# Kernel tuning notes

Hardware: AMD Instinct MI355X
Metric: run time of the kernel (lower is better)

The kernel has to match this reference:

```python
import jax, jax.numpy as jnp
import numpy as np

D_MODEL = 512
OUT_MODEL = 512
NUM_HEADS = 8
D_K = OUT_MODEL // NUM_HEADS


def setup_inputs() -> dict:
    key = jax.random.key(0)
    ks = jax.random.split(key, 11)
    B, S = 4, 2048
    inp = {
        "Q": jax.random.normal(ks[0], (B, S, D_MODEL), dtype=jnp.float32),
        "K": jax.random.normal(ks[1], (B, S, D_MODEL), dtype=jnp.float32),
        "V": jax.random.normal(ks[2], (B, S, D_MODEL), dtype=jnp.float32),
    }
    sc = 1.0 / np.sqrt(D_MODEL)
    inp["Wq"] = jax.random.normal(ks[3], (D_MODEL, OUT_MODEL), dtype=jnp.float32) * sc
    inp["bq"] = jnp.zeros((OUT_MODEL,), dtype=jnp.float32)
    inp["Wk"] = jax.random.normal(ks[4], (D_MODEL, OUT_MODEL), dtype=jnp.float32) * sc
    inp["bk"] = jnp.zeros((OUT_MODEL,), dtype=jnp.float32)
    inp["Wv"] = jax.random.normal(ks[5], (D_MODEL, OUT_MODEL), dtype=jnp.float32) * sc
    inp["bv"] = jnp.zeros((OUT_MODEL,), dtype=jnp.float32)
    inp["Wo"] = jax.random.normal(ks[6], (OUT_MODEL, OUT_MODEL), dtype=jnp.float32) * sc
    inp["bo"] = jnp.zeros((OUT_MODEL,), dtype=jnp.float32)
    return inp


def _split_heads(x):
    B, S, _ = x.shape
    return x.reshape(B, S, NUM_HEADS, D_K).transpose(0, 2, 1, 3)  # [B,H,S,Dk]


def reference(Q, K, V, Wq, bq, Wk, bk, Wv, bv, Wo, bo):
    q = _split_heads(Q @ Wq + bq)
    k = _split_heads(K @ Wk + bk)
    v = _split_heads(V @ Wv + bv)
    scores = jnp.einsum("bhsd,bhtd->bhst", q, k) / jnp.sqrt(jnp.float32(D_K))
    probs = jax.nn.softmax(scores, axis=-1)
    attn = jnp.einsum("bhst,bhtd->bhsd", probs, v)  # [B,H,S,Dk]
    B, H, S, Dk = attn.shape
    merged = attn.transpose(0, 2, 1, 3).reshape(B, S, OUT_MODEL)
    return merged @ Wo + bo
```

## Files before the change

### kernel.cpp

```cpp
#include <hip/hip_runtime.h>
#include <hip/hip_bf16.h>
#include <cstdint>


using short8 = __attribute__((ext_vector_type(8))) short;
using f32x4  = __attribute__((ext_vector_type(4))) float;
using f32x16 = __attribute__((ext_vector_type(16))) float;

#define DEVINL __device__ __forceinline__

constexpr int BB  = 4;
constexpr int SS  = 2048;
constexpr int DM  = 512;
constexpr int NH  = 8;
constexpr int DKH = 64;
constexpr float C2 = 0.18033688011112042f;

DEVINL unsigned short f2bf(float f) {
    __hip_bfloat16 h = __float2bfloat16(f);
    return *reinterpret_cast<unsigned short*>(&h);
}

DEVINL f32x4 mfma16(short8 a, short8 b, f32x4 c) {
    return __builtin_amdgcn_mfma_f32_16x16x32_bf16(a, b, c, 0, 0, 0);
}
DEVINL f32x16 mfma32(short8 a, short8 b, f32x16 c) {
    return __builtin_amdgcn_mfma_f32_32x32x16_bf16(a, b, c, 0, 0, 0);
}

DEVINL void gl16(const void* g, void* l) {
    __builtin_amdgcn_global_load_lds(
        (const __attribute__((address_space(1))) unsigned int*)g,
        (__attribute__((address_space(3))) unsigned int*)l, 16, 0, 0);
}
DEVINL void vmcnt0() { asm volatile("s_waitcnt vmcnt(0)" ::: "memory"); }

DEVINL unsigned cvtpk(float a, float b) {
    unsigned r;
    asm("v_cvt_pk_bf16_f32 %0, %1, %2" : "=v"(r) : "v"(a), "v"(b));
    return r;
}

__global__ __launch_bounds__(256)
void prep_w(const float* __restrict__ Wq, const float* __restrict__ Wk,
            const float* __restrict__ Wv, const float* __restrict__ Wo,
            unsigned short* __restrict__ wt)
{
    const int z = blockIdx.z;
    const float* W = (z == 0) ? Wq : (z == 1) ? Wk : (z == 2) ? Wv : Wo;
    unsigned short* Wtz = wt + (size_t)z * DM * DM;

    __shared__ unsigned short T[64][72];
    const int t = threadIdx.x;
    const int k0 = blockIdx.x * 64, n0 = blockIdx.y * 64;
    const int r = t >> 2, cs = t & 3;

    #pragma unroll
    for (int q = 0; q < 4; ++q) {
        float4 v = *reinterpret_cast<const float4*>(
            &W[(size_t)(k0 + r) * DM + n0 + cs * 16 + q * 4]);
        union { unsigned short u[4]; unsigned long long ll; } pk;
        pk.u[0] = f2bf(v.x); pk.u[1] = f2bf(v.y);
        pk.u[2] = f2bf(v.z); pk.u[3] = f2bf(v.w);
        *reinterpret_cast<unsigned long long*>(&T[r][cs * 16 + q * 4]) = pk.ll;
    }
    __syncthreads();
    union { unsigned short u[8]; short8 v; } p0, p1;
    #pragma unroll
    for (int e = 0; e < 8; ++e) p0.u[e] = T[cs * 16 + e][r];
    #pragma unroll
    for (int e = 0; e < 8; ++e) p1.u[e] = T[cs * 16 + 8 + e][r];
    *reinterpret_cast<short8*>(&Wtz[(size_t)(n0 + r) * DM + k0 + cs * 16]) = p0.v;
    *reinterpret_cast<short8*>(&Wtz[(size_t)(n0 + r) * DM + k0 + cs * 16 + 8]) = p1.v;
}

__global__ __launch_bounds__(256, 4)
void qkv_proj_kernel(const float* __restrict__ Qin, const float* __restrict__ Kin,
                     const float* __restrict__ Vin,
                     const unsigned short* __restrict__ wt,
                     const float* __restrict__ bq, const float* __restrict__ bk,
                     const float* __restrict__ bv,
                     unsigned short* __restrict__ qb, unsigned short* __restrict__ kb2,
                     unsigned short* __restrict__ vt2)
{
    const int z = blockIdx.z;
    const float* A           = (z == 0) ? Qin : (z == 1) ? Kin : Vin;
    const unsigned short* Wt = wt + (size_t)z * DM * DM;
    const float* bias        = (z == 0) ? bq : (z == 1) ? bk : bv;

    __shared__ unsigned short SMEM[16384];

    const int tid = threadIdx.x, lane = tid & 63, w = tid >> 6;
    const int wm = w >> 1, wn = w & 1;
    const int row16 = lane & 15, kg = lane >> 4;
    const int m0tok = blockIdx.x * 128, n0ch = blockIdx.y * 128;

    const int ar = tid >> 1, ah = tid & 1;

    float4 apf[4];
    auto load_A = [&](int kt) {
        const float* Ap = &A[(size_t)(m0tok + ar) * DM + kt * 32 + ah * 16];
        #pragma unroll
        for (int q = 0; q < 4; ++q)
            apf[q] = *reinterpret_cast<const float4*>(Ap + q * 4);
    };
    auto write_A = [&](int buf) {
        #pragma unroll
        for (int s = 0; s < 2; ++s) {
            union { unsigned short u[8]; short8 v; } pk;
            float4 a = apf[2 * s], b = apf[2 * s + 1];
            pk.u[0] = f2bf(a.x); pk.u[1] = f2bf(a.y);
            pk.u[2] = f2bf(a.z); pk.u[3] = f2bf(a.w);
            pk.u[4] = f2bf(b.x); pk.u[5] = f2bf(b.y);
            pk.u[6] = f2bf(b.z); pk.u[7] = f2bf(b.w);
            int phys = (ah * 2 + s) ^ (ar & 3);
            *reinterpret_cast<short8*>(&SMEM[buf * 4096 + ar * 32 + phys * 8]) = pk.v;
        }
    };
    auto issue_B = [&](int kt, int buf) {
        #pragma unroll
        for (int i = 0; i < 2; ++i) {
            int chunk = tid + i * 256;
            int n = chunk >> 2, c = chunk & 3;
            const unsigned short* src =
                &Wt[(size_t)(n0ch + n) * DM + kt * 32 + ((c ^ (n & 3)) * 8)];
            gl16(src, (char*)SMEM + 16384 + (size_t)buf * 8192 +
                      (size_t)(w * 64 + i * 256) * 16);
        }
    };

    f32x4 acc[4][4] = {};
    const int aoff = ((z == 2) ? wn : wm) * 64;
    const int boff = ((z == 2) ? wm : wn) * 64;

    load_A(0); issue_B(0, 0);
    vmcnt0();
    write_A(0);
    __syncthreads();

    for (int t = 0; t < 16; ++t) {
        const int cur = t & 1, nxt = cur ^ 1;
        if (t + 1 < 16) { issue_B(t + 1, nxt); load_A(t + 1); }

        short8 af[4], bfr[4];
        #pragma unroll
        for (int i = 0; i < 4; ++i) {
            int ra = aoff + i * 16 + row16;
            int rb = boff + i * 16 + row16;
            af[i]  = *reinterpret_cast<const short8*>(
                &SMEM[cur * 4096 + ra * 32 + ((kg ^ (ra & 3)) * 8)]);
            bfr[i] = *reinterpret_cast<const short8*>(
                &SMEM[8192 + cur * 4096 + rb * 32 + ((kg ^ (rb & 3)) * 8)]);
        }
        __builtin_amdgcn_s_setprio(1);
        #pragma unroll
        for (int mf = 0; mf < 4; ++mf)
            #pragma unroll
            for (int nf = 0; nf < 4; ++nf)
                acc[mf][nf] = (z == 2)
                    ? mfma16(bfr[mf], af[nf], acc[mf][nf])
                    : mfma16(af[mf], bfr[nf], acc[mf][nf]);
        __builtin_amdgcn_s_setprio(0);

        vmcnt0();
        if (t + 1 < 16) write_A(nxt);
        __syncthreads();
    }

    if (z == 0) {
        #pragma unroll
        for (int nf = 0; nf < 4; ++nf) {
            int ch = n0ch + wn * 64 + nf * 16 + row16;
            float bval = bias[ch];
            int h = ch >> 6, dk = ch & 63;
            #pragma unroll
            for (int mf = 0; mf < 4; ++mf)
                #pragma unroll
                for (int j = 0; j < 4; ++j) {
                    int tok = m0tok + wm * 64 + mf * 16 + kg * 4 + j;
                    int b = tok >> 11, s = tok & 2047;
                    qb[(((size_t)b * NH + h) * SS + s) * DKH + dk] =
                        f2bf((acc[mf][nf][j] + bval) * C2);
                }
        }
    } else {
        __syncthreads();
        if (z == 1) {
            #pragma unroll
            for (int nf = 0; nf < 4; ++nf) {
                int dk = nf * 16 + row16;
                float bval = bias[n0ch + wn * 64 + dk];
                #pragma unroll
                for (int mf = 0; mf < 4; ++mf)
                    #pragma unroll
                    for (int j = 0; j < 4; ++j) {
                        int s6 = mf * 16 + kg * 4 + j;
                        SMEM[w * 4096 + (dk >> 3) * 512 + s6 * 8 + (dk & 7)] =
                            f2bf(acc[mf][nf][j] + bval);
                    }
            }
        } else {
            const int tile = wn * 2 + wm;
            #pragma unroll
            for (int mf = 0; mf < 4; ++mf)
                #pragma unroll
                for (int j = 0; j < 4; ++j) {
                    int dk6 = mf * 16 + kg * 4 + j;
                    float bval = bias[n0ch + wm * 64 + dk6];
                    #pragma unroll
                    for (int nf = 0; nf < 4; ++nf) {
                        int s6 = nf * 16 + row16;
                        SMEM[tile * 4096 + (s6 >> 3) * 512 + dk6 * 8 + (s6 & 7)] =
                            f2bf(acc[mf][nf][j] + bval);
                    }
                }
        }
        __syncthreads();
        const int sblk = m0tok + (w >> 1) * 64;
        const int hg   = (n0ch >> 6) + (w & 1);
        const int b    = sblk >> 11, s_in_b = sblk & 2047;
        unsigned short* dst =
            ((z == 1) ? kb2 : vt2) +
            ((size_t)(b * NH + hg)) * (SS * DKH) + (size_t)(s_in_b >> 6) * 4096;
        #pragma unroll
        for (int i = 0; i < 8; ++i)
            *reinterpret_cast<short8*>(&dst[i * 512 + lane * 8]) =
                *reinterpret_cast<const short8*>(&SMEM[w * 4096 + i * 512 + lane * 8]);
    }
}

__global__ __launch_bounds__(256, 4)
void attn_kernel(const unsigned short* __restrict__ qb,
                 const unsigned short* __restrict__ kb2,
                 const unsigned short* __restrict__ vt2,
                 unsigned short* __restrict__ am)
{
    __shared__ unsigned short Ks[2][4096];
    __shared__ unsigned short Vs[3][4096];

    const int tid = threadIdx.x, lane = tid & 63, w = tid >> 6;
    const int l31 = lane & 31, hi = lane >> 5;
    const int bh = blockIdx.y, b = bh >> 3, h = bh & 7;
    const int q0 = blockIdx.x * 128;
    const size_t base = (size_t)bh * (SS * DKH);

    auto stage_KV = [&](int tt) {
        const unsigned short* ksrc = kb2 + base + (size_t)tt * 4096;
        const unsigned short* vsrc = vt2 + base + (size_t)tt * 4096;
        const int kbuf = tt & 1, vbuf = tt % 3;
        #pragma unroll
        for (int i = 0; i < 2; ++i) {
            int cb = i * 256 + w * 64;
            gl16(ksrc + (size_t)(cb + lane) * 8, (char*)Ks[kbuf] + (size_t)cb * 16);
            gl16(vsrc + (size_t)(cb + lane) * 8, (char*)Vs[vbuf] + (size_t)cb * 16);
        }
    };

    short8 qf[4];
    const int qrow = q0 + w * 32 + l31;
    #pragma unroll
    for (int ks = 0; ks < 4; ++ks)
        qf[ks] = *reinterpret_cast<const short8*>(
            &qb[base + (size_t)qrow * DKH + (ks * 2 + hi) * 8]);
    vmcnt0();

    stage_KV(0);
    __syncthreads();

    f32x16 o[2] = {};
    float lsum = 0.f;
    unsigned pk[2][4][2];

    auto do_QK = [&](int kcur, f32x16 (&sfr)[2]) {
        #pragma unroll
        for (int ks = 0; ks < 4; ++ks) {
            int c = ks * 2 + hi;
            #pragma unroll
            for (int mkv = 0; mkv < 2; ++mkv) {
                short8 kf = *reinterpret_cast<const short8*>(
                    &Ks[kcur][(c * 64 + mkv * 32 + l31) * 8]);
                sfr[mkv] = mfma32(kf, qf[ks], sfr[mkv]);
            }
        }
    };
    auto do_softmax = [&](const f32x16 (&sfr)[2]) {
        #pragma unroll
        for (int mkv = 0; mkv < 2; ++mkv)
            #pragma unroll
            for (int bq = 0; bq < 4; ++bq) {
                float p0 = __builtin_amdgcn_exp2f(sfr[mkv][bq * 4 + 0]);
                float p1 = __builtin_amdgcn_exp2f(sfr[mkv][bq * 4 + 1]);
                float p2 = __builtin_amdgcn_exp2f(sfr[mkv][bq * 4 + 2]);
                float p3 = __builtin_amdgcn_exp2f(sfr[mkv][bq * 4 + 3]);
                lsum += (p0 + p1) + (p2 + p3);
                pk[mkv][bq][0] = cvtpk(p0, p1);
                pk[mkv][bq][1] = cvtpk(p2, p3);
            }
    };
    auto do_PV = [&](int vbuf) {
        #pragma unroll
        for (int ks2 = 0; ks2 < 4; ++ks2) {
            const int mkv = ks2 >> 1, b0 = (ks2 & 1) * 2, b1 = b0 + 1;
            unsigned x0 = pk[mkv][b0][0], y0 = pk[mkv][b1][0];
            unsigned x1 = pk[mkv][b0][1], y1 = pk[mkv][b1][1];
            asm volatile("v_permlane32_swap_b32 %0, %1" : "+v"(x0), "+v"(y0));
            asm volatile("v_permlane32_swap_b32 %0, %1" : "+v"(x1), "+v"(y1));
            union { unsigned u[4]; short8 s; } pa;
            pa.u[0] = x0; pa.u[1] = x1; pa.u[2] = y0; pa.u[3] = y1;
            int c = ks2 * 2 + hi;
            #pragma unroll
            for (int ndk = 0; ndk < 2; ++ndk) {
                short8 vf = *reinterpret_cast<const short8*>(
                    &Vs[vbuf][(c * 64 + ndk * 32 + l31) * 8]);
                o[ndk] = mfma32(pa.s, vf, o[ndk]);
            }
        }
    };

    {
        stage_KV(1);
        f32x16 sfr[2] = {};
        __builtin_amdgcn_s_setprio(1);
        do_QK(0, sfr);
        __builtin_amdgcn_s_setprio(0);
        do_softmax(sfr);
        __syncthreads();
    }

    for (int tt = 1; tt < 32; ++tt) {
        if (tt < 31) stage_KV(tt + 1);

        f32x16 sfr[2] = {};
        __builtin_amdgcn_s_setprio(1);
        do_QK(tt & 1, sfr);
        do_PV((tt - 1) % 3);
        __builtin_amdgcn_s_setprio(0);
        do_softmax(sfr);

        if (tt < 31) __syncthreads();
    }
    do_PV(31 % 3);

    float lfull = lsum + __shfl_xor(lsum, 32, 64);
    float linv = 1.0f / lfull;
    #pragma unroll
    for (int r = 0; r < 16; ++r) {
        int qloc = (r & 3) + 8 * (r >> 2) + 4 * hi;
        float li = __shfl(linv, qloc, 64);
        int sg = q0 + w * 32 + qloc;
        #pragma unroll
        for (int ndk = 0; ndk < 2; ++ndk) {
            int dk = ndk * 32 + l31;
            am[((size_t)b * SS + sg) * DM + h * DKH + dk] =
                f2bf(o[ndk][r] * li);
        }
    }
}

__global__ __launch_bounds__(256, 4)
void out_proj_kernel(const unsigned short* __restrict__ am,
                     const unsigned short* __restrict__ Wt,
                     const float* __restrict__ bo,
                     float* __restrict__ out)
{
    __shared__ unsigned short As[2][64 * 32];
    __shared__ unsigned short Bs[2][128 * 32];

    const int tid = threadIdx.x, lane = tid & 63, w = tid >> 6;
    const int wm = w & 1, wn = w >> 1;
    const int row16 = lane & 15, kg = lane >> 4;
    const int m0 = blockIdx.x * 64;
    const int n0 = blockIdx.y * 128;

    auto stage = [&](int kt, int buf) {
        {
            int r = tid >> 2, c = tid & 3;
            gl16(&am[(size_t)(m0 + r) * DM + kt * 32 + ((c ^ (r & 3)) * 8)],
                 (char*)As + (size_t)buf * 4096 + (size_t)(w * 64) * 16);
        }
        #pragma unroll
        for (int i = 0; i < 2; ++i) {
            int cc = tid + i * 256;
            int n = cc >> 2, c = cc & 3;
            gl16(&Wt[(size_t)(n0 + n) * DM + kt * 32 + ((c ^ (n & 3)) * 8)],
                 (char*)Bs + (size_t)buf * 8192 + (size_t)(w * 64 + i * 256) * 16);
        }
    };

    f32x4 acc[2][4] = {};

    stage(0, 0);
    vmcnt0();
    __syncthreads();

    for (int t = 0; t < 16; ++t) {
        const int cur = t & 1, nxt = cur ^ 1;
        if (t + 1 < 16) stage(t + 1, nxt);

        short8 af[2], bfr[4];
        #pragma unroll
        for (int i = 0; i < 2; ++i) {
            int ra = wm * 32 + i * 16 + row16;
            af[i] = *reinterpret_cast<const short8*>(
                &As[cur][ra * 32 + ((kg ^ (ra & 3)) * 8)]);
        }
        #pragma unroll
        for (int i = 0; i < 4; ++i) {
            int rb = wn * 64 + i * 16 + row16;
            bfr[i] = *reinterpret_cast<const short8*>(
                &Bs[cur][rb * 32 + ((kg ^ (rb & 3)) * 8)]);
        }
        __builtin_amdgcn_s_setprio(1);
        #pragma unroll
        for (int mf = 0; mf < 2; ++mf)
            #pragma unroll
            for (int nf = 0; nf < 4; ++nf)
                acc[mf][nf] = mfma16(af[mf], bfr[nf], acc[mf][nf]);
        __builtin_amdgcn_s_setprio(0);

        vmcnt0();
        __syncthreads();
    }

    #pragma unroll
    for (int nf = 0; nf < 4; ++nf) {
        int n = n0 + wn * 64 + nf * 16 + row16;
        float bval = bo[n];
        #pragma unroll
        for (int mf = 0; mf < 2; ++mf)
            #pragma unroll
            for (int j = 0; j < 4; ++j) {
                int mrow = m0 + wm * 32 + mf * 16 + kg * 4 + j;
                out[(size_t)mrow * DM + n] = acc[mf][nf][j] + bval;
            }
    }
}

extern "C" void kernel_launch(void* const* d_in, const int* in_sizes, int n_in,
                              void* d_out, int out_size, void* d_ws, size_t ws_size,
                              hipStream_t stream) {
    const float* Q  = (const float*)d_in[0];
    const float* K  = (const float*)d_in[1];
    const float* V  = (const float*)d_in[2];
    const float* Wq = (const float*)d_in[3];
    const float* bq = (const float*)d_in[4];
    const float* Wk = (const float*)d_in[5];
    const float* bk = (const float*)d_in[6];
    const float* Wv = (const float*)d_in[7];
    const float* bv = (const float*)d_in[8];
    const float* Wo = (const float*)d_in[9];
    const float* bo = (const float*)d_in[10];
    float* out = (float*)d_out;

    const size_t per = (size_t)BB * NH * SS * DKH;
    unsigned short* qb  = (unsigned short*)d_ws;
    unsigned short* kb2 = qb + per;
    unsigned short* vt2 = kb2 + per;
    unsigned short* am  = vt2 + per;
    unsigned short* wt  = am + per;

    prep_w<<<dim3(8, 8, 4), 256, 0, stream>>>(Wq, Wk, Wv, Wo, wt);
    qkv_proj_kernel<<<dim3(64, 4, 3), 256, 0, stream>>>(
        Q, K, V, wt, bq, bk, bv, qb, kb2, vt2);
    attn_kernel<<<dim3(SS / 128, BB * NH), 256, 0, stream>>>(qb, kb2, vt2, am);
    out_proj_kernel<<<dim3(128, 4), 256, 0, stream>>>(
        am, wt + 3 * (size_t)DM * DM, bo, out);
}
```

Measured before the change: 87.81 us.

## Load K tiles directly into registers and restructure attention pipeline

K tiles are now loaded from global memory straight into registers (double-buffered kA/kB) instead of being staged through shared memory. V stays in LDS but drops from triple to double buffering. The loop is unrolled by two and no longer runs the P·V of the previous tile alongside the current Q·K; each tile does QK, softmax and PV in order. Launch bounds drop to 2 blocks per SM, which frees registers for the K fragments but may lower occupancy. The overlap between QK and the previous PV is lost, and per-wave K loads are duplicated across the four waves.

```diff
diff --git a/kernel.cpp b/kernel.cpp
--- a/kernel.cpp
+++ b/kernel.cpp
@@ -229,14 +229,13 @@
     }
 }
 
-__global__ __launch_bounds__(256, 4)
+__global__ __launch_bounds__(256, 2)
 void attn_kernel(const unsigned short* __restrict__ qb,
                  const unsigned short* __restrict__ kb2,
                  const unsigned short* __restrict__ vt2,
                  unsigned short* __restrict__ am)
 {
-    __shared__ unsigned short Ks[2][4096];
-    __shared__ unsigned short Vs[3][4096];
+    __shared__ unsigned short Vs[2][4096];
 
     const int tid = threadIdx.x, lane = tid & 63, w = tid >> 6;
     const int l31 = lane & 31, hi = lane >> 5;
@@ -244,15 +243,24 @@
     const int q0 = blockIdx.x * 128;
     const size_t base = (size_t)bh * (SS * DKH);
 
-    auto stage_KV = [&](int tt) {
-        const unsigned short* ksrc = kb2 + base + (size_t)tt * 4096;
+    auto stage_V = [&](int tt) {
         const unsigned short* vsrc = vt2 + base + (size_t)tt * 4096;
-        const int kbuf = tt & 1, vbuf = tt % 3;
+        const int buf = tt & 1;
         #pragma unroll
         for (int i = 0; i < 2; ++i) {
             int cb = i * 256 + w * 64;
-            gl16(ksrc + (size_t)(cb + lane) * 8, (char*)Ks[kbuf] + (size_t)cb * 16);
-            gl16(vsrc + (size_t)(cb + lane) * 8, (char*)Vs[vbuf] + (size_t)cb * 16);
+            gl16(vsrc + (size_t)(cb + lane) * 8, (char*)Vs[buf] + (size_t)cb * 16);
+        }
+    };
+    auto load_K = [&](int tt, short8 (&kr)[8]) {
+        const unsigned short* ksrc = kb2 + base + (size_t)tt * 4096;
+        #pragma unroll
+        for (int ks = 0; ks < 4; ++ks) {
+            int c = ks * 2 + hi;
+            #pragma unroll
+            for (int mkv = 0; mkv < 2; ++mkv)
+                kr[ks * 2 + mkv] = *reinterpret_cast<const short8*>(
+                    &ksrc[(c * 64 + mkv * 32 + l31) * 8]);
         }
     };
 
@@ -262,27 +270,18 @@
     for (int ks = 0; ks < 4; ++ks)
         qf[ks] = *reinterpret_cast<const short8*>(
             &qb[base + (size_t)qrow * DKH + (ks * 2 + hi) * 8]);
-    vmcnt0();
-
-    stage_KV(0);
-    __syncthreads();
 
     f32x16 o[2] = {};
     float lsum = 0.f;
+
+    auto do_QK = [&](const short8 (&kr)[8], f32x16 (&sfr)[2]) {
+        #pragma unroll
+        for (int ks = 0; ks < 4; ++ks)
+            #pragma unroll
+            for (int mkv = 0; mkv < 2; ++mkv)
+                sfr[mkv] = mfma32(kr[ks * 2 + mkv], qf[ks], sfr[mkv]);
+    };
     unsigned pk[2][4][2];
-
-    auto do_QK = [&](int kcur, f32x16 (&sfr)[2]) {
-        #pragma unroll
-        for (int ks = 0; ks < 4; ++ks) {
-            int c = ks * 2 + hi;
-            #pragma unroll
-            for (int mkv = 0; mkv < 2; ++mkv) {
-                short8 kf = *reinterpret_cast<const short8*>(
-                    &Ks[kcur][(c * 64 + mkv * 32 + l31) * 8]);
-                sfr[mkv] = mfma32(kf, qf[ks], sfr[mkv]);
-            }
-        }
-    };
     auto do_softmax = [&](const f32x16 (&sfr)[2]) {
         #pragma unroll
         for (int mkv = 0; mkv < 2; ++mkv)
@@ -317,29 +316,41 @@
         }
     };
 
-    {
-        stage_KV(1);
-        f32x16 sfr[2] = {};
-        __builtin_amdgcn_s_setprio(1);
-        do_QK(0, sfr);
-        __builtin_amdgcn_s_setprio(0);
-        do_softmax(sfr);
+    short8 kA[8], kB[8];
+    load_K(0, kA);
+    stage_V(0);
+    __syncthreads();
+
+    for (int p = 0; p < 16; ++p) {
+        const int tE = 2 * p, tO = 2 * p + 1;
+
+        load_K(tO, kB);
+        stage_V(tO);
+        {
+            f32x16 sfr[2] = {};
+            __builtin_amdgcn_s_setprio(1);
+            do_QK(kA, sfr);
+            __builtin_amdgcn_s_setprio(0);
+            do_softmax(sfr);
+            __builtin_amdgcn_s_setprio(1);
+            do_PV(0);
+            __builtin_amdgcn_s_setprio(0);
+        }
         __syncthreads();
-    }
-
-    for (int tt = 1; tt < 32; ++tt) {
-        if (tt < 31) stage_KV(tt + 1);
-
-        f32x16 sfr[2] = {};
-        __builtin_amdgcn_s_setprio(1);
-        do_QK(tt & 1, sfr);
-        do_PV((tt - 1) % 3);
-        __builtin_amdgcn_s_setprio(0);
-        do_softmax(sfr);
-
-        if (tt < 31) __syncthreads();
-    }
-    do_PV(31 % 3);
+
+        if (p < 15) { load_K(tO + 1, kA); stage_V(tO + 1); }
+        {
+            f32x16 sfr[2] = {};
+            __builtin_amdgcn_s_setprio(1);
+            do_QK(kB, sfr);
+            __builtin_amdgcn_s_setprio(0);
+            do_softmax(sfr);
+            __builtin_amdgcn_s_setprio(1);
+            do_PV(1);
+            __builtin_amdgcn_s_setprio(0);
+        }
+        if (p < 15) __syncthreads();
+    }
 
     float lfull = lsum + __shfl_xor(lsum, 32, 64);
     float linv = 1.0f / lfull;
```

After: 92.30 us. +5.1%, slower.

## Split KV sequence across two wave groups in attention block and combine

Applied to the files above, without the earlier changes.

The attention kernel now uses 512 threads per block. Two groups of four waves each process half of the key/value tiles (16 each) for the same 128 queries, and their partial outputs and row sums are merged through shared memory at the end. The per-group pipeline also drops the QK/PV software overlap and the triple V buffer in favour of simple double buffering. This doubles the waves per block, aiming for more latency hiding and shorter serial loops. The cost is an extra LDS reduction pass and the loss of the QK/PV overlap within each wave.

```diff
diff --git a/kernel.cpp b/kernel.cpp
--- a/kernel.cpp
+++ b/kernel.cpp
@@ -229,35 +229,39 @@
     }
 }
 
-__global__ __launch_bounds__(256, 4)
+__global__ __launch_bounds__(512, 4)
 void attn_kernel(const unsigned short* __restrict__ qb,
                  const unsigned short* __restrict__ kb2,
                  const unsigned short* __restrict__ vt2,
                  unsigned short* __restrict__ am)
 {
-    __shared__ unsigned short Ks[2][4096];
-    __shared__ unsigned short Vs[3][4096];
+    __shared__ unsigned short Ks[2][2][4096];
+    __shared__ unsigned short Vs[2][2][4096];
 
     const int tid = threadIdx.x, lane = tid & 63, w = tid >> 6;
+    const int wq = w & 3, hf = w >> 2;
     const int l31 = lane & 31, hi = lane >> 5;
     const int bh = blockIdx.y, b = bh >> 3, h = bh & 7;
     const int q0 = blockIdx.x * 128;
     const size_t base = (size_t)bh * (SS * DKH);
-
-    auto stage_KV = [&](int tt) {
+    const int tile0 = hf * 16;
+
+    auto stage_KV = [&](int tl) {
+        const int tt = tile0 + tl, buf = tl & 1;
         const unsigned short* ksrc = kb2 + base + (size_t)tt * 4096;
         const unsigned short* vsrc = vt2 + base + (size_t)tt * 4096;
-        const int kbuf = tt & 1, vbuf = tt % 3;
         #pragma unroll
         for (int i = 0; i < 2; ++i) {
-            int cb = i * 256 + w * 64;
-            gl16(ksrc + (size_t)(cb + lane) * 8, (char*)Ks[kbuf] + (size_t)cb * 16);
-            gl16(vsrc + (size_t)(cb + lane) * 8, (char*)Vs[vbuf] + (size_t)cb * 16);
+            int cb = i * 256 + wq * 64;
+            gl16(ksrc + (size_t)(cb + lane) * 8,
+                 (char*)Ks[hf][buf] + (size_t)cb * 16);
+            gl16(vsrc + (size_t)(cb + lane) * 8,
+                 (char*)Vs[hf][buf] + (size_t)cb * 16);
         }
     };
 
     short8 qf[4];
-    const int qrow = q0 + w * 32 + l31;
+    const int qrow = q0 + wq * 32 + l31;
     #pragma unroll
     for (int ks = 0; ks < 4; ++ks)
         qf[ks] = *reinterpret_cast<const short8*>(
@@ -271,14 +275,14 @@
     float lsum = 0.f;
     unsigned pk[2][4][2];
 
-    auto do_QK = [&](int kcur, f32x16 (&sfr)[2]) {
+    auto do_QK = [&](int buf, f32x16 (&sfr)[2]) {
         #pragma unroll
         for (int ks = 0; ks < 4; ++ks) {
             int c = ks * 2 + hi;
             #pragma unroll
             for (int mkv = 0; mkv < 2; ++mkv) {
                 short8 kf = *reinterpret_cast<const short8*>(
-                    &Ks[kcur][(c * 64 + mkv * 32 + l31) * 8]);
+                    &Ks[hf][buf][(c * 64 + mkv * 32 + l31) * 8]);
                 sfr[mkv] = mfma32(kf, qf[ks], sfr[mkv]);
             }
         }
@@ -297,7 +301,7 @@
                 pk[mkv][bq][1] = cvtpk(p2, p3);
             }
     };
-    auto do_PV = [&](int vbuf) {
+    auto do_PV = [&](int buf) {
         #pragma unroll
         for (int ks2 = 0; ks2 < 4; ++ks2) {
             const int mkv = ks2 >> 1, b0 = (ks2 & 1) * 2, b1 = b0 + 1;
@@ -311,48 +315,60 @@
             #pragma unroll
             for (int ndk = 0; ndk < 2; ++ndk) {
                 short8 vf = *reinterpret_cast<const short8*>(
-                    &Vs[vbuf][(c * 64 + ndk * 32 + l31) * 8]);
+                    &Vs[hf][buf][(c * 64 + ndk * 32 + l31) * 8]);
                 o[ndk] = mfma32(pa.s, vf, o[ndk]);
             }
         }
     };
 
-    {
-        stage_KV(1);
+    for (int tl = 0; tl < 16; ++tl) {
+        if (tl < 15) stage_KV(tl + 1);
+        const int buf = tl & 1;
+
         f32x16 sfr[2] = {};
         __builtin_amdgcn_s_setprio(1);
-        do_QK(0, sfr);
+        do_QK(buf, sfr);
         __builtin_amdgcn_s_setprio(0);
         do_softmax(sfr);
-        __syncthreads();
-    }
-
-    for (int tt = 1; tt < 32; ++tt) {
-        if (tt < 31) stage_KV(tt + 1);
-
-        f32x16 sfr[2] = {};
         __builtin_amdgcn_s_setprio(1);
-        do_QK(tt & 1, sfr);
-        do_PV((tt - 1) % 3);
+        do_PV(buf);
         __builtin_amdgcn_s_setprio(0);
-        do_softmax(sfr);
-
-        if (tt < 31) __syncthreads();
-    }
-    do_PV(31 % 3);
-
-    float lfull = lsum + __shfl_xor(lsum, 32, 64);
-    float linv = 1.0f / lfull;
-    #pragma unroll
-    for (int r = 0; r < 16; ++r) {
-        int qloc = (r & 3) + 8 * (r >> 2) + 4 * hi;
-        float li = __shfl(linv, qloc, 64);
-        int sg = q0 + w * 32 + qloc;
-        #pragma unroll
-        for (int ndk = 0; ndk < 2; ++ndk) {
-            int dk = ndk * 32 + l31;
-            am[((size_t)b * SS + sg) * DM + h * DKH + dk] =
-                f2bf(o[ndk][r] * li);
+
+        if (tl < 15) __syncthreads();
+    }
+
+    __syncthreads();
+    float* comb  = reinterpret_cast<float*>(&Ks[0][0][0]);
+    float* lcomb = reinterpret_cast<float*>(&Vs[0][0][0]);
+    if (hf == 1) {
+        #pragma unroll
+        for (int ndk = 0; ndk < 2; ++ndk)
+            #pragma unroll
+            for (int r = 0; r < 16; ++r)
+                comb[((wq * 2 + ndk) * 16 + r) * 64 + lane] = o[ndk][r];
+        lcomb[wq * 64 + lane] = lsum;
+    }
+    __syncthreads();
+    if (hf == 0) {
+        lsum += lcomb[wq * 64 + lane];
+        float lfull = lsum + __shfl_xor(lsum, 32, 64);
+        float linv = 1.0f / lfull;
+        #pragma unroll
+        for (int ndk = 0; ndk < 2; ++ndk)
+            #pragma unroll
+            for (int r = 0; r < 16; ++r)
+                o[ndk][r] += comb[((wq * 2 + ndk) * 16 + r) * 64 + lane];
+        #pragma unroll
+        for (int r = 0; r < 16; ++r) {
+            int qloc = (r & 3) + 8 * (r >> 2) + 4 * hi;
+            float li = __shfl(linv, qloc, 64);
+            int sg = q0 + wq * 32 + qloc;
+            #pragma unroll
+            for (int ndk = 0; ndk < 2; ++ndk) {
+                int dk = ndk * 32 + l31;
+                am[((size_t)b * SS + sg) * DM + h * DKH + dk] =
+                    f2bf(o[ndk][r] * li);
+            }
         }
     }
 }
@@ -462,7 +478,7 @@
     prep_w<<<dim3(8, 8, 4), 256, 0, stream>>>(Wq, Wk, Wv, Wo, wt);
     qkv_proj_kernel<<<dim3(64, 4, 3), 256, 0, stream>>>(
         Q, K, V, wt, bq, bk, bv, qb, kb2, vt2);
-    attn_kernel<<<dim3(SS / 128, BB * NH), 256, 0, stream>>>(qb, kb2, vt2, am);
+    attn_kernel<<<dim3(SS / 128, BB * NH), 512, 0, stream>>>(qb, kb2, vt2, am);
     out_proj_kernel<<<dim3(128, 4), 256, 0, stream>>>(
         am, wt + 3 * (size_t)DM * DM, bo, out);
 }
```

Result: no change. 87.53 us (median of 2 runs) (-0.3%).
